# Kernel tuning notes

Measured on AMD Instinct MI355X. Metric: run time of the kernel, lower is better.

The kernel has to match this reference:

```python
import jax, jax.numpy as jnp
import numpy as np

D, T, HID, Q = 33, 49, 64, 64


def _lin(x, w, b):
    return x @ w.T + b


def setup_inputs() -> dict:
    key = jax.random.key(0)
    ks = jax.random.split(key, 40)

    def nrm(k, shape, scale=0.1):
        return jax.random.normal(k, shape, jnp.float32) * scale

    vals = nrm(ks[0], (D, T), 1.0)
    mask = (jax.random.uniform(ks[1], (D, T)) < 0.8).astype(jnp.float32)
    delta = jax.random.uniform(ks[2], (D, T)) * 2.0
    data = jnp.stack([vals, mask, delta])  # [3, 33, 49]

    return {
        "data": data,
        "h0": nrm(ks[3], (HID,), 1.0),
        "H0": nrm(ks[4], (D, HID), 1.0),
        "gh_w": nrm(ks[5], (HID, D)), "gh_b": nrm(ks[6], (HID,)),
        "gst_w": nrm(ks[7], (HID, D)), "gst_b": nrm(ks[8], (HID,)),
        "gru_wih": nrm(ks[9], (3 * HID, D)), "gru_whh": nrm(ks[10], (3 * HID, HID)),
        "gru_bih": nrm(ks[11], (3 * HID,)), "gru_bhh": nrm(ks[12], (3 * HID,)),
        "wu0_w": nrm(ks[13], (Q, HID)), "wu0_b": nrm(ks[14], (Q,)),
        "wu1_w": nrm(ks[15], (Q, 2 * HID)), "wu1_b": nrm(ks[16], (Q,)),
        "wu_w": nrm(ks[17], (Q, 3 * HID)), "wu_b": nrm(ks[18], (Q,)),
        "wh_w": nrm(ks[19], (D, HID + Q)), "wh_b": nrm(ks[20], (D,)),
        "xst_w": nrm(ks[21], (1, HID)), "xst_b": nrm(ks[22], (1,)),
        "wrg_w": nrm(ks[23], (D, HID)),
        "wrs": nrm(ks[24], (1, HID)),
        "tWz": nrm(ks[25], (D, HID, HID)), "tUzx": nrm(ks[26], (D, HID, 1)), "tUzh": nrm(ks[27], (D, HID, HID)),
        "tWr": nrm(ks[28], (D, HID, HID)), "tUrx": nrm(ks[29], (D, HID, 1)), "tUrh": nrm(ks[30], (D, HID, HID)),
        "tWh": nrm(ks[31], (D, HID, HID)), "tUhx": nrm(ks[32], (D, HID, 1)), "tUhh": nrm(ks[33], (D, HID, HID)),
        "tbz": nrm(ks[34], (HID, 1)), "tbr": nrm(ks[35], (HID, 1)), "tbh": nrm(ks[36], (HID, 1)),
    }


def reference(data, h0, H0, gh_w, gh_b, gst_w, gst_b, gru_wih, gru_whh,
              gru_bih, gru_bhh, wu0_w, wu0_b, wu1_w, wu1_b, wu_w, wu_b,
              wh_w, wh_b, xst_w, xst_b, wrg_w, wrs, tWz, tUzx, tUzh,
              tWr, tUrx, tUrh, tWh, tUhx, tUhh, tbz, tbr, tbh):
    X, M, Dt = data[0], data[1], data[2]  # each (33, 49)
    h = h0          # (HID,) -> becomes (1, HID) after first GRUCell step
    H = H0          # (D, HID)
    outs, Hs, xps = [], [], []
    for t in range(T):
        x, m, d = X[:, t], M[:, t], Dt[:, t]
        # GRU-D style decay gate: exp(-max(0, Linear(delta)))
        gamma_h = jnp.exp(-jax.nn.relu(_lin(d, gh_w, gh_b)))
        h = gamma_h * h
        x_st = _lin(H, xst_w, xst_b).reshape(-1)       # (D,)
        x_st_c = m * x + (1 - m) * x_st                # imputed input
        # torch nn.GRUCell
        xi = x_st_c.reshape(1, D)
        hi = h.reshape(1, HID)
        gi = _lin(xi, gru_wih, gru_bih)
        gh_ = _lin(hi, gru_whh, gru_bhh)
        i_r, i_z, i_n = jnp.split(gi, 3, axis=1)
        h_r, h_z, h_n = jnp.split(gh_, 3, axis=1)
        r = jax.nn.sigmoid(i_r + h_r)
        z = jax.nn.sigmoid(i_z + h_z)
        n = jnp.tanh(i_n + r * h_n)
        h = (1 - z) * n + z * hi                       # (1, HID)
        # original detaches the history used for u_t
        outs.append(jax.lax.stop_gradient(h))
        if t == 0:
            u_t = _lin(h0.reshape(1, -1), wu0_w, wu0_b)
        elif t == 1:
            hd = jnp.concatenate([h0.reshape(1, -1), outs[0]], 0).reshape(1, -1)
            u_t = _lin(hd, wu1_w, wu1_b)
        elif t == 2:
            hd = jnp.concatenate([h0.reshape(1, -1), outs[0], outs[1]], 0).reshape(1, -1)
            u_t = _lin(hd, wu_w, wu_b)
        else:
            hd = jnp.concatenate(outs[t - 3:t], 0).reshape(1, -1)
            u_t = _lin(hd, wu_w, wu_b)
        x_gt_hat = _lin(jnp.concatenate([h, u_t], axis=1), wh_w, wh_b)  # (1, D)
        gamma_st = jnp.exp(-jax.nn.relu(_lin(d, gst_w, gst_b)))
        H = gamma_st * H
        # tMGRU cell: per-variable (D=33) batched matmuls
        Hr = H[:, :, None]              # (D, HID, 1)
        xr = x_st_c[:, None, None]      # (D, 1, 1)
        hr = h.reshape(HID, 1)          # (HID, 1)
        z_t = jax.nn.sigmoid(tWz @ Hr + tUzx @ xr + tUzh @ hr + tbz)
        r_t = jax.nn.sigmoid(tWr @ Hr + tUrx @ xr + tUrh @ hr + tbr)
        Hh = jnp.tanh(r_t * (tWh @ Hr) + tUhx @ xr + tUhh @ hr + tbh)
        H = (z_t * Hr + (1 - z_t) * Hh).reshape(D, HID)
        Hs.append(H)
        a = h @ wrg_w.T                 # (1, D)
        b = wrs @ H.T                   # (1, D)
        alpha1 = jax.nn.softmax(a / (a + b), axis=-1)
        alpha2 = jax.nn.softmax(b / (a + b), axis=-1)
        xps.append(alpha1 * x_gt_hat + alpha2 * x_st)  # (1, D)
    H_s = jnp.stack(Hs)                         # (T, D, HID)
    x_pred = jnp.concatenate(xps, axis=0).T     # (D, T)
    return H_s, x_pred
```

## Files before the change

### kernel.cpp

```cpp
#include <hip/hip_runtime.h>
#include <math.h>

#define DD 33
#define TT 49
#define HH 64
#define NB 33
#define NT 256

#define O_WIHT  0
#define O_WHHT  6336
#define O_GH    18624
#define O_GS    21760
#define O_WT0   24896
#define O_WT1   27008
#define O_WTG   31232
#define O_CU    37568
#define O_XC    37700
#define O_R     39317
#define O_FLAGS 42560
#define PREP_N  37700

#define SC_AGENT __HIP_MEMORY_SCOPE_AGENT

__device__ __forceinline__ float sigm(float x) { return 1.f / (1.f + expf(-x)); }

__device__ __forceinline__ float rsum64(float v) {
#pragma unroll
  for (int o = 32; o > 0; o >>= 1) v += __shfl_xor(v, o, 64);
  return v;
}
__device__ __forceinline__ float rmax64(float v) {
#pragma unroll
  for (int o = 32; o > 0; o >>= 1) v = fmaxf(v, __shfl_xor(v, o, 64));
  return v;
}

extern "C" __global__ void gmgru_prep(
    const float* __restrict__ data, const float* __restrict__ gh_w,
    const float* __restrict__ gh_b, const float* __restrict__ gst_w,
    const float* __restrict__ gst_b, const float* __restrict__ wih,
    const float* __restrict__ whh, const float* __restrict__ wu0,
    const float* __restrict__ wu0b, const float* __restrict__ wu1,
    const float* __restrict__ wu1b, const float* __restrict__ wu,
    const float* __restrict__ wub, const float* __restrict__ wh_w,
    float* __restrict__ ws) {
  int idx = blockIdx.x * blockDim.x + threadIdx.x;
  if (idx < 6336) {
    int k = idx / 192, j = idx % 192;
    ws[O_WIHT + idx] = wih[j * DD + k];
  } else if (idx < 18624) {
    int r = idx - 6336, k = r / 192, j = r % 192;
    ws[O_WHHT + r] = whh[j * HH + k];
  } else if (idx < 21760) {
    int r = idx - 18624, t = r / 64, i = r % 64;
    float s = gh_b[i];
    for (int d2 = 0; d2 < DD; ++d2)
      s += data[2 * DD * TT + d2 * TT + t] * gh_w[i * DD + d2];
    ws[O_GH + r] = expf(-fmaxf(s, 0.f));
  } else if (idx < 24896) {
    int r = idx - 21760, t = r / 64, i = r % 64;
    float s = gst_b[i];
    for (int d2 = 0; d2 < DD; ++d2)
      s += data[2 * DD * TT + d2 * TT + t] * gst_w[i * DD + d2];
    ws[O_GS + r] = expf(-fmaxf(s, 0.f));
  } else if (idx < 27008) {
    int r = idx - 24896, dd = r / 64, k = r % 64;
    float s = 0.f;
    for (int q = 0; q < 64; ++q) s += wu0[q * 64 + k] * wh_w[dd * 128 + 64 + q];
    ws[O_WT0 + r] = s;
  } else if (idx < 31232) {
    int r = idx - 27008, dd = r / 128, k = r % 128;
    float s = 0.f;
    for (int q = 0; q < 64; ++q) s += wu1[q * 128 + k] * wh_w[dd * 128 + 64 + q];
    ws[O_WT1 + r] = s;
  } else if (idx < 37568) {
    int r = idx - 31232, dd = r / 192, k = r % 192;
    float s = 0.f;
    for (int q = 0; q < 64; ++q) s += wu[q * 192 + k] * wh_w[dd * 128 + 64 + q];
    ws[O_WTG + r] = s;
  } else if (idx < PREP_N) {
    int r = idx - 37568, dd = r / 4, v = r % 4;
    float s = 0.f;
    if (v < 3) {
      const float* bp = (v == 0) ? wu0b : (v == 1) ? wu1b : wub;
      for (int q = 0; q < 64; ++q) s += bp[q] * wh_w[dd * 128 + 64 + q];
    }
    ws[O_CU + r] = s;
  }
}

extern "C" __global__ void __launch_bounds__(NT)
gmgru_main(const float* __restrict__ data, const float* __restrict__ h0,
           const float* __restrict__ H0, const float* __restrict__ bih,
           const float* __restrict__ bhh, const float* __restrict__ wh_w,
           const float* __restrict__ wh_b, const float* __restrict__ xst_w,
           const float* __restrict__ xst_b, const float* __restrict__ wrg_w,
           const float* __restrict__ wrs, const float* __restrict__ tWz,
           const float* __restrict__ tUzx, const float* __restrict__ tUzh,
           const float* __restrict__ tWr, const float* __restrict__ tUrx,
           const float* __restrict__ tUrh, const float* __restrict__ tWh,
           const float* __restrict__ tUhx, const float* __restrict__ tUhh,
           const float* __restrict__ tbz, const float* __restrict__ tbr,
           const float* __restrict__ tbh, float* __restrict__ ws,
           unsigned* __restrict__ flags, float* __restrict__ out) {
  __shared__ __attribute__((aligned(16))) float ubuf[3][4096];
  __shared__ float whhT_l[12288];
  __shared__ float wihT_l[6336];
  __shared__ float partW[3][4][HH], partU[3][4][HH];
  __shared__ float ux[3][HH], tbl[3][HH];
  __shared__ float Hrow[HH], Hdec[HH], hpre[HH], hprev[HH], hnew_l[HH], h0s[HH];
  __shared__ float hist[4][HH];
  __shared__ float ghL[3 * HH];
  __shared__ float bihL[3 * HH], bhhL[3 * HH];
  __shared__ float whr0[HH], wtgL[192], wt0L[HH], wt1L[128];
  __shared__ float wrgr[HH], wrsr[HH], xstwL[HH];
  __shared__ float xrow[TT], mrow[TT];
  __shared__ float gpre[2][HH];
  __shared__ float scal2[2][2];

  const int tid = threadIdx.x;
  const int dd = blockIdx.x;
  const int wid = tid >> 6;
  const int lane = tid & 63;

  {
    const float* usrc[3] = {tUzh, tUrh, tUhh};
#pragma unroll 1
    for (int m = 0; m < 3; ++m) {
      const float* s = usrc[m] + dd * 4096;
#pragma unroll
      for (int c = 0; c < 4; ++c) {
        int f = tid * 16 + c * 4;
        float4 v = *reinterpret_cast<const float4*>(s + f);
        int i = f >> 6, k = f & 63;
        *reinterpret_cast<float4*>(&ubuf[m][(k >> 2) * 256 + i * 4]) = v;
      }
    }
  }
  for (int i = tid; i < 12288; i += NT) whhT_l[i] = ws[O_WHHT + i];
  for (int i = tid; i < 6336; i += NT) wihT_l[i] = ws[O_WIHT + i];
  if (tid < 192) {
    bihL[tid] = bih[tid];
    bhhL[tid] = bhh[tid];
    wtgL[tid] = ws[O_WTG + dd * 192 + tid];
  }
  if (tid < 128) wt1L[tid] = ws[O_WT1 + dd * 128 + tid];
  if (tid < HH) {
    ux[0][tid] = tUzx[dd * HH + tid];
    ux[1][tid] = tUrx[dd * HH + tid];
    ux[2][tid] = tUhx[dd * HH + tid];
    tbl[0][tid] = tbz[tid];
    tbl[1][tid] = tbr[tid];
    tbl[2][tid] = tbh[tid];
    Hrow[tid] = H0[dd * HH + tid];
    float h0v = h0[tid];
    h0s[tid] = h0v;
    hprev[tid] = h0v;
    whr0[tid] = wh_w[dd * 128 + tid];
    wt0L[tid] = ws[O_WT0 + dd * 64 + tid];
    wrgr[tid] = wrg_w[dd * HH + tid];
    wrsr[tid] = wrs[tid];
    xstwL[tid] = xst_w[tid];
    gpre[0][tid] = ws[O_GH + tid];
    gpre[1][tid] = ws[O_GS + tid];
  }
  if (tid < TT) {
    xrow[tid] = data[dd * TT + tid];
    mrow[tid] = data[DD * TT + dd * TT + tid];
  }
  const float whb_r = wh_b[dd];
  const float xstb_r = xst_b[0];
  const float cu0_r = ws[O_CU + dd * 4 + 0];
  const float cu1_r = ws[O_CU + dd * 4 + 1];
  const float cu2_r = ws[O_CU + dd * 4 + 2];
  __syncthreads();

  float xst_cur = 0.f;
  if (wid == 0) {
    float s = rsum64(Hrow[lane] * xstwL[lane]);
    if (lane == 0) {
      float xstv = s + xstb_r;
      xst_cur = xstv;
      float xcv = mrow[0] * xrow[0] + (1.f - mrow[0]) * xstv;
      __hip_atomic_store(&ws[O_XC + dd], xcv, __ATOMIC_RELAXED, SC_AGENT);
      asm volatile("s_waitcnt vmcnt(0)" ::: "memory");
      __hip_atomic_store(&flags[dd], 1u, __ATOMIC_RELAXED, SC_AGENT);
    }
  }

  for (int t = 0; t < TT; ++t) {
    __syncthreads();
    if (tid < HH) {
      hpre[tid] = gpre[0][tid] * hprev[tid];
      Hdec[tid] = gpre[1][tid] * Hrow[tid];
    }
    __syncthreads();

    {
      float Hv[16];
#pragma unroll
      for (int j = 0; j < 16; ++j) Hv[j] = Hdec[wid * 16 + j];
      float pw0 = 0.f, pw1 = 0.f, pw2 = 0.f;
      const int base = dd * 4096 + lane * 64 + wid * 16;
#pragma unroll
      for (int g = 0; g < 4; ++g) {
        float4 a = *reinterpret_cast<const float4*>(tWz + base + g * 4);
        float4 b = *reinterpret_cast<const float4*>(tWr + base + g * 4);
        float4 c = *reinterpret_cast<const float4*>(tWh + base + g * 4);
        const float h0v = Hv[g * 4 + 0], h1v = Hv[g * 4 + 1];
        const float h2v = Hv[g * 4 + 2], h3v = Hv[g * 4 + 3];
        pw0 += a.x * h0v + a.y * h1v + a.z * h2v + a.w * h3v;
        pw1 += b.x * h0v + b.y * h1v + b.z * h2v + b.w * h3v;
        pw2 += c.x * h0v + c.y * h1v + c.z * h2v + c.w * h3v;
      }
      partW[0][wid][lane] = pw0;
      partW[1][wid][lane] = pw1;
      partW[2][wid][lane] = pw2;
    }
    if (tid < 3 * HH) {
      float a0 = 0.f, a1 = 0.f, a2 = 0.f, a3 = 0.f;
#pragma unroll
      for (int k = 0; k < HH; k += 4) {
        a0 += whhT_l[(k + 0) * 192 + tid] * hpre[k + 0];
        a1 += whhT_l[(k + 1) * 192 + tid] * hpre[k + 1];
        a2 += whhT_l[(k + 2) * 192 + tid] * hpre[k + 2];
        a3 += whhT_l[(k + 3) * 192 + tid] * hpre[k + 3];
      }
      ghL[tid] = bhhL[tid] + ((a0 + a1) + (a2 + a3));
    }

    float hn = 0.f, xcv_reg = 0.f;
    if (wid == 0) {
      const unsigned tgt = (unsigned)(t + 1);
      while (true) {
        unsigned v = (lane < NB)
            ? __hip_atomic_load(&flags[lane], __ATOMIC_RELAXED, SC_AGENT)
            : 0xFFFFFFFFu;
        if (__all((int)(v >= tgt))) break;
        __builtin_amdgcn_s_sleep(1);
      }
      asm volatile("" ::: "memory");
      float xcv = 0.f;
      if (lane < DD)
        xcv = __hip_atomic_load(&ws[O_XC + t * DD + lane], __ATOMIC_RELAXED,
                                SC_AGENT);
      xcv_reg = xcv;
      float gr = bihL[lane], gz = bihL[64 + lane], gn = bihL[128 + lane];
      for (int k = 0; k < DD; ++k) {
        float xk = __shfl(xcv, k, 64);
        gr += wihT_l[k * 192 + lane] * xk;
        gz += wihT_l[k * 192 + 64 + lane] * xk;
        gn += wihT_l[k * 192 + 128 + lane] * xk;
      }
      float r = sigm(gr + ghL[lane]);
      float z = sigm(gz + ghL[64 + lane]);
      float n = tanhf(gn + r * ghL[128 + lane]);
      hn = (1.f - z) * n + z * hpre[lane];
      hnew_l[lane] = hn;
      hist[t & 3][lane] = hn;
      hprev[lane] = hn;
    }
    __syncthreads();

    {
      float hv[16];
#pragma unroll
      for (int j = 0; j < 16; ++j) hv[j] = hnew_l[wid * 16 + j];
      float pu0 = 0.f, pu1 = 0.f, pu2 = 0.f;
#pragma unroll
      for (int g = 0; g < 4; ++g) {
        const int kg = (wid * 4 + g) * 256 + lane * 4;
        float4 a = *reinterpret_cast<const float4*>(&ubuf[0][kg]);
        float4 b = *reinterpret_cast<const float4*>(&ubuf[1][kg]);
        float4 c = *reinterpret_cast<const float4*>(&ubuf[2][kg]);
        const float h0v = hv[g * 4 + 0], h1v = hv[g * 4 + 1];
        const float h2v = hv[g * 4 + 2], h3v = hv[g * 4 + 3];
        pu0 += a.x * h0v + a.y * h1v + a.z * h2v + a.w * h3v;
        pu1 += b.x * h0v + b.y * h1v + b.z * h2v + b.w * h3v;
        pu2 += c.x * h0v + c.y * h1v + c.z * h2v + c.w * h3v;
      }
      partU[0][wid][lane] = pu0;
      partU[1][wid][lane] = pu1;
      partU[2][wid][lane] = pu2;
    }
    __syncthreads();

    if (wid == 0) {
      float sz = partW[0][0][lane] + partW[0][1][lane] + partW[0][2][lane] +
                 partW[0][3][lane] + partU[0][0][lane] + partU[0][1][lane] +
                 partU[0][2][lane] + partU[0][3][lane];
      float sr = partW[1][0][lane] + partW[1][1][lane] + partW[1][2][lane] +
                 partW[1][3][lane] + partU[1][0][lane] + partU[1][1][lane] +
                 partU[1][2][lane] + partU[1][3][lane];
      float swh = partW[2][0][lane] + partW[2][1][lane] + partW[2][2][lane] +
                  partW[2][3][lane];
      float suh = partU[2][0][lane] + partU[2][1][lane] + partU[2][2][lane] +
                  partU[2][3][lane];
      float xc = __shfl(xcv_reg, dd, 64);
      float z = sigm(sz + ux[0][lane] * xc + tbl[0][lane]);
      float r = sigm(sr + ux[1][lane] * xc + tbl[1][lane]);
      float hh = tanhf(r * swh + ux[2][lane] * xc + suh + tbl[2][lane]);
      float Hn = z * Hdec[lane] + (1.f - z) * hh;
      Hrow[lane] = Hn;
      out[t * DD * HH + dd * HH + lane] = Hn;
      float xg = whr0[lane] * hn;
      if (t == 0) {
        xg += wt0L[lane] * h0s[lane];
      } else if (t == 1) {
        xg += wt1L[lane] * h0s[lane] + wt1L[64 + lane] * hist[0][lane];
      } else if (t == 2) {
        xg += wtgL[lane] * h0s[lane] + wtgL[64 + lane] * hist[0][lane] +
              wtgL[128 + lane] * hist[1][lane];
      } else {
        const int s0 = (t - 3) & 3, s1 = (t - 2) & 3, s2 = (t - 1) & 3;
        xg += wtgL[lane] * hist[s0][lane] + wtgL[64 + lane] * hist[s1][lane] +
              wtgL[128 + lane] * hist[s2][lane];
      }
      float xgt = rsum64(xg);
      float av = rsum64(wrgr[lane] * hn);
      float bv = rsum64(wrsr[lane] * Hn);
      float xsn = rsum64(xstwL[lane] * Hn);
      if (lane == 0) {
        float cu = (t == 0) ? cu0_r : (t == 1) ? cu1_r : cu2_r;
        scal2[t & 1][0] = xgt + whb_r + cu;
        scal2[t & 1][1] = xst_cur;
        float s = av + bv;
        __hip_atomic_store(&ws[O_R + t * 66 + dd], av / s, __ATOMIC_RELAXED,
                           SC_AGENT);
        __hip_atomic_store(&ws[O_R + t * 66 + 33 + dd], bv / s,
                           __ATOMIC_RELAXED, SC_AGENT);
        if (t < TT - 1) {
          float xstv = xsn + xstb_r;
          float xcn = mrow[t + 1] * xrow[t + 1] + (1.f - mrow[t + 1]) * xstv;
          __hip_atomic_store(&ws[O_XC + (t + 1) * DD + dd], xcn,
                             __ATOMIC_RELAXED, SC_AGENT);
          xst_cur = xstv;
        }
        asm volatile("s_waitcnt vmcnt(0)" ::: "memory");
        __hip_atomic_store(&flags[dd], (unsigned)(t + 2), __ATOMIC_RELAXED,
                           SC_AGENT);
      }
    } else if (wid == 1) {
      if (t > 0) {
        float r1v = -INFINITY, r2v = -INFINITY;
        if (lane < DD) {
          r1v = __hip_atomic_load(&ws[O_R + (t - 1) * 66 + lane],
                                  __ATOMIC_RELAXED, SC_AGENT);
          r2v = __hip_atomic_load(&ws[O_R + (t - 1) * 66 + 33 + lane],
                                  __ATOMIC_RELAXED, SC_AGENT);
        }
        float m1 = rmax64(r1v), m2 = rmax64(r2v);
        float e1 = (lane < DD) ? expf(r1v - m1) : 0.f;
        float e2 = (lane < DD) ? expf(r2v - m2) : 0.f;
        float s1 = rsum64(e1), s2 = rsum64(e2);
        float r1o = __shfl(r1v, dd, 64);
        float r2o = __shfl(r2v, dd, 64);
        if (lane == 0) {
          float a1 = expf(r1o - m1) / s1;
          float a2 = expf(r2o - m2) / s2;
          out[TT * DD * HH + dd * TT + (t - 1)] =
              a1 * scal2[(t - 1) & 1][0] + a2 * scal2[(t - 1) & 1][1];
        }
      }
    } else if (wid == 2) {
      if (t + 1 < TT) {
        gpre[0][lane] = ws[O_GH + (t + 1) * HH + lane];
        gpre[1][lane] = ws[O_GS + (t + 1) * HH + lane];
      }
    }
  }

  if (wid == 0) {
    const unsigned tgt = (unsigned)(TT + 1);
    while (true) {
      unsigned v = (lane < NB)
          ? __hip_atomic_load(&flags[lane], __ATOMIC_RELAXED, SC_AGENT)
          : 0xFFFFFFFFu;
      if (__all((int)(v >= tgt))) break;
      __builtin_amdgcn_s_sleep(1);
    }
    asm volatile("" ::: "memory");
  }
  __syncthreads();
  if (wid == 1) {
    float r1v = -INFINITY, r2v = -INFINITY;
    if (lane < DD) {
      r1v = __hip_atomic_load(&ws[O_R + (TT - 1) * 66 + lane], __ATOMIC_RELAXED,
                              SC_AGENT);
      r2v = __hip_atomic_load(&ws[O_R + (TT - 1) * 66 + 33 + lane],
                              __ATOMIC_RELAXED, SC_AGENT);
    }
    float m1 = rmax64(r1v), m2 = rmax64(r2v);
    float e1 = (lane < DD) ? expf(r1v - m1) : 0.f;
    float e2 = (lane < DD) ? expf(r2v - m2) : 0.f;
    float s1 = rsum64(e1), s2 = rsum64(e2);
    float r1o = __shfl(r1v, dd, 64);
    float r2o = __shfl(r2v, dd, 64);
    if (lane == 0) {
      float a1 = expf(r1o - m1) / s1;
      float a2 = expf(r2o - m2) / s2;
      out[TT * DD * HH + dd * TT + (TT - 1)] =
          a1 * scal2[(TT - 1) & 1][0] + a2 * scal2[(TT - 1) & 1][1];
    }
  }
}

extern "C" void kernel_launch(void* const* d_in, const int* in_sizes, int n_in,
                              void* d_out, int out_size, void* d_ws,
                              size_t ws_size, hipStream_t stream) {
  (void)in_sizes; (void)n_in; (void)out_size; (void)ws_size;
  const float* data   = (const float*)d_in[0];
  const float* h0     = (const float*)d_in[1];
  const float* H0     = (const float*)d_in[2];
  const float* gh_w   = (const float*)d_in[3];
  const float* gh_b   = (const float*)d_in[4];
  const float* gst_w  = (const float*)d_in[5];
  const float* gst_b  = (const float*)d_in[6];
  const float* wih    = (const float*)d_in[7];
  const float* whh    = (const float*)d_in[8];
  const float* bih    = (const float*)d_in[9];
  const float* bhh    = (const float*)d_in[10];
  const float* wu0w   = (const float*)d_in[11];
  const float* wu0b   = (const float*)d_in[12];
  const float* wu1w   = (const float*)d_in[13];
  const float* wu1b   = (const float*)d_in[14];
  const float* wuw    = (const float*)d_in[15];
  const float* wub    = (const float*)d_in[16];
  const float* wh_w   = (const float*)d_in[17];
  const float* wh_b   = (const float*)d_in[18];
  const float* xst_w  = (const float*)d_in[19];
  const float* xst_b  = (const float*)d_in[20];
  const float* wrg_w  = (const float*)d_in[21];
  const float* wrs    = (const float*)d_in[22];
  const float* tWz    = (const float*)d_in[23];
  const float* tUzx   = (const float*)d_in[24];
  const float* tUzh   = (const float*)d_in[25];
  const float* tWr    = (const float*)d_in[26];
  const float* tUrx   = (const float*)d_in[27];
  const float* tUrh   = (const float*)d_in[28];
  const float* tWh    = (const float*)d_in[29];
  const float* tUhx   = (const float*)d_in[30];
  const float* tUhh   = (const float*)d_in[31];
  const float* tbz    = (const float*)d_in[32];
  const float* tbr    = (const float*)d_in[33];
  const float* tbh    = (const float*)d_in[34];

  float* ws = (float*)d_ws;
  unsigned* flags = (unsigned*)(ws + O_FLAGS);

  hipMemsetAsync(flags, 0, 64 * sizeof(unsigned), stream);
  gmgru_prep<<<(PREP_N + 255) / 256, 256, 0, stream>>>(
      data, gh_w, gh_b, gst_w, gst_b, wih, whh, wu0w, wu0b, wu1w, wu1b, wuw,
      wub, wh_w, ws);
  gmgru_main<<<NB, NT, 0, stream>>>(
      data, h0, H0, bih, bhh, wh_w, wh_b, xst_w, xst_b, wrg_w, wrs, tWz, tUzx,
      tUzh, tWr, tUrx, tUrh, tWh, tUhx, tUhh, tbz, tbr, tbh, ws, flags,
      (float*)d_out);
}
```

Before: 220.5 us.

## Pack value and tag into 64-bit flags and keep per-step state in registers

Replaces the separate flag array plus value store with one 64-bit word per step per block that carries both the tag and the value. A single relaxed atomic load now both synchronises and delivers the data, so the separate fence and flag store disappear. The GRU cell is computed redundantly by every wave, with state held in registers and shuffles instead of shared memory, which cuts a __syncthreads per step. The softmax output is delayed by one extra step so its wait on remote data overlaps other work. It also preloads all gamma values into LDS, reads W_hh from global memory instead of LDS, and switches to fast exp/tanh, trading some accuracy and more global traffic for lower latency on the critical path.

```diff
diff --git a/kernel.cpp b/kernel.cpp
--- a/kernel.cpp
+++ b/kernel.cpp
@@ -15,14 +15,20 @@
 #define O_WT1   27008
 #define O_WTG   31232
 #define O_CU    37568
-#define O_XC    37700
-#define O_R     39317
-#define O_FLAGS 42560
+#define O_R     37700
+#define O_PF    40936
 #define PREP_N  37700
 
 #define SC_AGENT __HIP_MEMORY_SCOPE_AGENT
 
-__device__ __forceinline__ float sigm(float x) { return 1.f / (1.f + expf(-x)); }
+__device__ __forceinline__ float sigm(float x) {
+  return 1.f / (1.f + __expf(-x));
+}
+__device__ __forceinline__ float ftanh(float x) {
+  x = fminf(fmaxf(x, -15.f), 15.f);
+  float e = __expf(2.f * x);
+  return (e - 1.f) / (e + 1.f);
+}
 
 __device__ __forceinline__ float rsum64(float v) {
 #pragma unroll
@@ -89,7 +95,7 @@
   }
 }
 
-extern "C" __global__ void __launch_bounds__(NT)
+extern "C" __global__ void __launch_bounds__(NT, 1)
 gmgru_main(const float* __restrict__ data, const float* __restrict__ h0,
            const float* __restrict__ H0, const float* __restrict__ bih,
            const float* __restrict__ bhh, const float* __restrict__ wh_w,
@@ -102,21 +108,14 @@
            const float* __restrict__ tUhx, const float* __restrict__ tUhh,
            const float* __restrict__ tbz, const float* __restrict__ tbr,
            const float* __restrict__ tbh, float* __restrict__ ws,
-           unsigned* __restrict__ flags, float* __restrict__ out) {
+           unsigned long long* __restrict__ pf, float* __restrict__ out) {
   __shared__ __attribute__((aligned(16))) float ubuf[3][4096];
-  __shared__ float whhT_l[12288];
   __shared__ float wihT_l[6336];
-  __shared__ float partW[3][4][HH], partU[3][4][HH];
-  __shared__ float ux[3][HH], tbl[3][HH];
-  __shared__ float Hrow[HH], Hdec[HH], hpre[HH], hprev[HH], hnew_l[HH], h0s[HH];
-  __shared__ float hist[4][HH];
-  __shared__ float ghL[3 * HH];
-  __shared__ float bihL[3 * HH], bhhL[3 * HH];
-  __shared__ float whr0[HH], wtgL[192], wt0L[HH], wt1L[128];
-  __shared__ float wrgr[HH], wrsr[HH], xstwL[HH];
+  __shared__ float gamH[TT * HH], gamS[TT * HH];
+  __shared__ float part[2][6][4][HH];
+  __shared__ float hpreL[HH];
+  __shared__ float ghLDS[3 * HH];
   __shared__ float xrow[TT], mrow[TT];
-  __shared__ float gpre[2][HH];
-  __shared__ float scal2[2][2];
 
   const int tid = threadIdx.x;
   const int dd = blockIdx.x;
@@ -137,270 +136,273 @@
       }
     }
   }
-  for (int i = tid; i < 12288; i += NT) whhT_l[i] = ws[O_WHHT + i];
   for (int i = tid; i < 6336; i += NT) wihT_l[i] = ws[O_WIHT + i];
-  if (tid < 192) {
-    bihL[tid] = bih[tid];
-    bhhL[tid] = bhh[tid];
-    wtgL[tid] = ws[O_WTG + dd * 192 + tid];
-  }
-  if (tid < 128) wt1L[tid] = ws[O_WT1 + dd * 128 + tid];
-  if (tid < HH) {
-    ux[0][tid] = tUzx[dd * HH + tid];
-    ux[1][tid] = tUrx[dd * HH + tid];
-    ux[2][tid] = tUhx[dd * HH + tid];
-    tbl[0][tid] = tbz[tid];
-    tbl[1][tid] = tbr[tid];
-    tbl[2][tid] = tbh[tid];
-    Hrow[tid] = H0[dd * HH + tid];
-    float h0v = h0[tid];
-    h0s[tid] = h0v;
-    hprev[tid] = h0v;
-    whr0[tid] = wh_w[dd * 128 + tid];
-    wt0L[tid] = ws[O_WT0 + dd * 64 + tid];
-    wrgr[tid] = wrg_w[dd * HH + tid];
-    wrsr[tid] = wrs[tid];
-    xstwL[tid] = xst_w[tid];
-    gpre[0][tid] = ws[O_GH + tid];
-    gpre[1][tid] = ws[O_GS + tid];
+  for (int i = tid; i < TT * HH; i += NT) {
+    gamH[i] = ws[O_GH + i];
+    gamS[i] = ws[O_GS + i];
   }
   if (tid < TT) {
     xrow[tid] = data[dd * TT + tid];
     mrow[tid] = data[DD * TT + dd * TT + tid];
   }
-  const float whb_r = wh_b[dd];
-  const float xstb_r = xst_b[0];
+  const float bih_r = bih[lane];
+  const float bih_z = bih[64 + lane];
+  const float bih_n = bih[128 + lane];
+  const float bhh_r = (tid < 192) ? bhh[tid] : 0.f;
+  const float ux0 = tUzx[dd * HH + lane];
+  const float ux1 = tUrx[dd * HH + lane];
+  const float ux2 = tUhx[dd * HH + lane];
+  const float tb0 = tbz[lane];
+  const float tb1 = tbr[lane];
+  const float tb2 = tbh[lane];
+  const float xstw_r = xst_w[lane];
+  const float wrg_r = wrg_w[dd * HH + lane];
+  const float wrs_r = wrs[lane];
+  const float whr0_r = wh_w[dd * 128 + lane];
+  const float wtg0_r = ws[O_WTG + dd * 192 + lane];
+  const float wtg1_r = ws[O_WTG + dd * 192 + 64 + lane];
+  const float wtg2_r = ws[O_WTG + dd * 192 + 128 + lane];
+  const float wt0_r = ws[O_WT0 + dd * 64 + lane];
+  const float wt1a_r = ws[O_WT1 + dd * 128 + lane];
+  const float wt1b_r = ws[O_WT1 + dd * 128 + 64 + lane];
   const float cu0_r = ws[O_CU + dd * 4 + 0];
   const float cu1_r = ws[O_CU + dd * 4 + 1];
   const float cu2_r = ws[O_CU + dd * 4 + 2];
+  const float whb_r = wh_b[dd];
+  const float xstb_r = xst_b[0];
+  const float h0s_r = h0[lane];
+  float hprev = h0s_r;
+  float Hrow = H0[dd * HH + lane];
   __syncthreads();
 
-  float xst_cur = 0.f;
-  if (wid == 0) {
-    float s = rsum64(Hrow[lane] * xstwL[lane]);
-    if (lane == 0) {
-      float xstv = s + xstb_r;
-      xst_cur = xstv;
-      float xcv = mrow[0] * xrow[0] + (1.f - mrow[0]) * xstv;
-      __hip_atomic_store(&ws[O_XC + dd], xcv, __ATOMIC_RELAXED, SC_AGENT);
-      asm volatile("s_waitcnt vmcnt(0)" ::: "memory");
-      __hip_atomic_store(&flags[dd], 1u, __ATOMIC_RELAXED, SC_AGENT);
-    }
-  }
+  float xst_cur = rsum64(Hrow * xstw_r) + xstb_r;
+  if (wid == 0 && lane == 0) {
+    float xc0 = mrow[0] * xrow[0] + (1.f - mrow[0]) * xst_cur;
+    unsigned long long pk0 =
+        (1ULL << 32) | (unsigned long long)__float_as_uint(xc0);
+    __hip_atomic_store(&pf[dd], pk0, __ATOMIC_RELAXED, SC_AGENT);
+  }
+  float xg_m1 = 0.f, xg_m2 = 0.f, xs_m1 = 0.f, xs_m2 = 0.f;
+  float h1 = 0.f, h2 = 0.f, h3 = 0.f;
 
   for (int t = 0; t < TT; ++t) {
+    const int b = t & 1;
+    float hpre_r = gamH[t * HH + lane] * hprev;
+    float Hdec_r = gamS[t * HH + lane] * Hrow;
+    if (wid == 0) hpreL[lane] = hpre_r;
     __syncthreads();
-    if (tid < HH) {
-      hpre[tid] = gpre[0][tid] * hprev[tid];
-      Hdec[tid] = gpre[1][tid] * Hrow[tid];
-    }
-    __syncthreads();
-
+    if (tid < 3 * HH) {
+      float a0 = 0.f, a1 = 0.f, a2 = 0.f, a3 = 0.f;
+#pragma unroll
+      for (int k = 0; k < HH; k += 4) {
+        a0 += ws[O_WHHT + (k + 0) * 192 + tid] * hpreL[k + 0];
+        a1 += ws[O_WHHT + (k + 1) * 192 + tid] * hpreL[k + 1];
+        a2 += ws[O_WHHT + (k + 2) * 192 + tid] * hpreL[k + 2];
+        a3 += ws[O_WHHT + (k + 3) * 192 + tid] * hpreL[k + 3];
+      }
+      ghLDS[tid] = bhh_r + ((a0 + a1) + (a2 + a3));
+    }
     {
-      float Hv[16];
-#pragma unroll
-      for (int j = 0; j < 16; ++j) Hv[j] = Hdec[wid * 16 + j];
       float pw0 = 0.f, pw1 = 0.f, pw2 = 0.f;
       const int base = dd * 4096 + lane * 64 + wid * 16;
 #pragma unroll
       for (int g = 0; g < 4; ++g) {
         float4 a = *reinterpret_cast<const float4*>(tWz + base + g * 4);
-        float4 b = *reinterpret_cast<const float4*>(tWr + base + g * 4);
+        float4 bb = *reinterpret_cast<const float4*>(tWr + base + g * 4);
         float4 c = *reinterpret_cast<const float4*>(tWh + base + g * 4);
-        const float h0v = Hv[g * 4 + 0], h1v = Hv[g * 4 + 1];
-        const float h2v = Hv[g * 4 + 2], h3v = Hv[g * 4 + 3];
-        pw0 += a.x * h0v + a.y * h1v + a.z * h2v + a.w * h3v;
-        pw1 += b.x * h0v + b.y * h1v + b.z * h2v + b.w * h3v;
-        pw2 += c.x * h0v + c.y * h1v + c.z * h2v + c.w * h3v;
-      }
-      partW[0][wid][lane] = pw0;
-      partW[1][wid][lane] = pw1;
-      partW[2][wid][lane] = pw2;
-    }
-    if (tid < 3 * HH) {
-      float a0 = 0.f, a1 = 0.f, a2 = 0.f, a3 = 0.f;
-#pragma unroll
-      for (int k = 0; k < HH; k += 4) {
-        a0 += whhT_l[(k + 0) * 192 + tid] * hpre[k + 0];
-        a1 += whhT_l[(k + 1) * 192 + tid] * hpre[k + 1];
-        a2 += whhT_l[(k + 2) * 192 + tid] * hpre[k + 2];
-        a3 += whhT_l[(k + 3) * 192 + tid] * hpre[k + 3];
-      }
-      ghL[tid] = bhhL[tid] + ((a0 + a1) + (a2 + a3));
-    }
-
-    float hn = 0.f, xcv_reg = 0.f;
-    if (wid == 0) {
-      const unsigned tgt = (unsigned)(t + 1);
-      while (true) {
-        unsigned v = (lane < NB)
-            ? __hip_atomic_load(&flags[lane], __ATOMIC_RELAXED, SC_AGENT)
-            : 0xFFFFFFFFu;
-        if (__all((int)(v >= tgt))) break;
+        float v0 = __shfl(Hdec_r, wid * 16 + g * 4 + 0, 64);
+        float v1 = __shfl(Hdec_r, wid * 16 + g * 4 + 1, 64);
+        float v2 = __shfl(Hdec_r, wid * 16 + g * 4 + 2, 64);
+        float v3 = __shfl(Hdec_r, wid * 16 + g * 4 + 3, 64);
+        pw0 += a.x * v0 + a.y * v1 + a.z * v2 + a.w * v3;
+        pw1 += bb.x * v0 + bb.y * v1 + bb.z * v2 + bb.w * v3;
+        pw2 += c.x * v0 + c.y * v1 + c.z * v2 + c.w * v3;
+      }
+      part[b][0][wid][lane] = pw0;
+      part[b][1][wid][lane] = pw1;
+      part[b][2][wid][lane] = pw2;
+    }
+    __syncthreads();
+
+    const unsigned tagv = (unsigned)(t + 1);
+    float xcv;
+    {
+      unsigned long long pk;
+      for (;;) {
+        pk = (lane < NB)
+                 ? __hip_atomic_load(&pf[(size_t)t * NB + lane],
+                                     __ATOMIC_RELAXED, SC_AGENT)
+                 : (((unsigned long long)tagv) << 32);
+        if (__all((int)((unsigned)(pk >> 32) == tagv))) break;
         __builtin_amdgcn_s_sleep(1);
       }
+      xcv = __uint_as_float((unsigned)(pk & 0xFFFFFFFFull));
       asm volatile("" ::: "memory");
-      float xcv = 0.f;
-      if (lane < DD)
-        xcv = __hip_atomic_load(&ws[O_XC + t * DD + lane], __ATOMIC_RELAXED,
-                                SC_AGENT);
-      xcv_reg = xcv;
-      float gr = bihL[lane], gz = bihL[64 + lane], gn = bihL[128 + lane];
-      for (int k = 0; k < DD; ++k) {
-        float xk = __shfl(xcv, k, 64);
-        gr += wihT_l[k * 192 + lane] * xk;
-        gz += wihT_l[k * 192 + 64 + lane] * xk;
-        gn += wihT_l[k * 192 + 128 + lane] * xk;
-      }
-      float r = sigm(gr + ghL[lane]);
-      float z = sigm(gz + ghL[64 + lane]);
-      float n = tanhf(gn + r * ghL[128 + lane]);
-      hn = (1.f - z) * n + z * hpre[lane];
-      hnew_l[lane] = hn;
-      hist[t & 3][lane] = hn;
-      hprev[lane] = hn;
-    }
-    __syncthreads();
+    }
+
+    float gr = bih_r, gz = bih_z, gn = bih_n;
+#pragma unroll
+    for (int k = 0; k < DD; ++k) {
+      float xk = __shfl(xcv, k, 64);
+      gr += wihT_l[k * 192 + lane] * xk;
+      gz += wihT_l[k * 192 + 64 + lane] * xk;
+      gn += wihT_l[k * 192 + 128 + lane] * xk;
+    }
+    float rg = sigm(gr + ghLDS[lane]);
+    float zg = sigm(gz + ghLDS[64 + lane]);
+    float ng = ftanh(gn + rg * ghLDS[128 + lane]);
+    float hn = (1.f - zg) * ng + zg * hpre_r;
 
     {
-      float hv[16];
-#pragma unroll
-      for (int j = 0; j < 16; ++j) hv[j] = hnew_l[wid * 16 + j];
       float pu0 = 0.f, pu1 = 0.f, pu2 = 0.f;
 #pragma unroll
       for (int g = 0; g < 4; ++g) {
         const int kg = (wid * 4 + g) * 256 + lane * 4;
         float4 a = *reinterpret_cast<const float4*>(&ubuf[0][kg]);
-        float4 b = *reinterpret_cast<const float4*>(&ubuf[1][kg]);
+        float4 bb = *reinterpret_cast<const float4*>(&ubuf[1][kg]);
         float4 c = *reinterpret_cast<const float4*>(&ubuf[2][kg]);
-        const float h0v = hv[g * 4 + 0], h1v = hv[g * 4 + 1];
-        const float h2v = hv[g * 4 + 2], h3v = hv[g * 4 + 3];
-        pu0 += a.x * h0v + a.y * h1v + a.z * h2v + a.w * h3v;
-        pu1 += b.x * h0v + b.y * h1v + b.z * h2v + b.w * h3v;
-        pu2 += c.x * h0v + c.y * h1v + c.z * h2v + c.w * h3v;
-      }
-      partU[0][wid][lane] = pu0;
-      partU[1][wid][lane] = pu1;
-      partU[2][wid][lane] = pu2;
+        float v0 = __shfl(hn, wid * 16 + g * 4 + 0, 64);
+        float v1 = __shfl(hn, wid * 16 + g * 4 + 1, 64);
+        float v2 = __shfl(hn, wid * 16 + g * 4 + 2, 64);
+        float v3 = __shfl(hn, wid * 16 + g * 4 + 3, 64);
+        pu0 += a.x * v0 + a.y * v1 + a.z * v2 + a.w * v3;
+        pu1 += bb.x * v0 + bb.y * v1 + bb.z * v2 + bb.w * v3;
+        pu2 += c.x * v0 + c.y * v1 + c.z * v2 + c.w * v3;
+      }
+      part[b][3][wid][lane] = pu0;
+      part[b][4][wid][lane] = pu1;
+      part[b][5][wid][lane] = pu2;
     }
     __syncthreads();
 
+    float r1v = -INFINITY, r2v = -INFINITY;
+    if (wid == 1 && t >= 2 && lane < DD) {
+      r1v = __hip_atomic_load(&ws[O_R + (t - 2) * 66 + lane], __ATOMIC_RELAXED,
+                              SC_AGENT);
+      r2v = __hip_atomic_load(&ws[O_R + (t - 2) * 66 + 33 + lane],
+                              __ATOMIC_RELAXED, SC_AGENT);
+    }
+
+    float sz = part[b][0][0][lane] + part[b][0][1][lane] + part[b][0][2][lane] +
+               part[b][0][3][lane] + part[b][3][0][lane] + part[b][3][1][lane] +
+               part[b][3][2][lane] + part[b][3][3][lane];
+    float sr = part[b][1][0][lane] + part[b][1][1][lane] + part[b][1][2][lane] +
+               part[b][1][3][lane] + part[b][4][0][lane] + part[b][4][1][lane] +
+               part[b][4][2][lane] + part[b][4][3][lane];
+    float swh = part[b][2][0][lane] + part[b][2][1][lane] +
+                part[b][2][2][lane] + part[b][2][3][lane];
+    float suh = part[b][5][0][lane] + part[b][5][1][lane] +
+                part[b][5][2][lane] + part[b][5][3][lane];
+    float xc = __shfl(xcv, dd, 64);
+    float z2 = sigm(sz + ux0 * xc + tb0);
+    float r2g = sigm(sr + ux1 * xc + tb1);
+    float hh = ftanh(r2g * swh + ux2 * xc + suh + tb2);
+    float Hn = z2 * Hdec_r + (1.f - z2) * hh;
+
     if (wid == 0) {
-      float sz = partW[0][0][lane] + partW[0][1][lane] + partW[0][2][lane] +
-                 partW[0][3][lane] + partU[0][0][lane] + partU[0][1][lane] +
-                 partU[0][2][lane] + partU[0][3][lane];
-      float sr = partW[1][0][lane] + partW[1][1][lane] + partW[1][2][lane] +
-                 partW[1][3][lane] + partU[1][0][lane] + partU[1][1][lane] +
-                 partU[1][2][lane] + partU[1][3][lane];
-      float swh = partW[2][0][lane] + partW[2][1][lane] + partW[2][2][lane] +
-                  partW[2][3][lane];
-      float suh = partU[2][0][lane] + partU[2][1][lane] + partU[2][2][lane] +
-                  partU[2][3][lane];
-      float xc = __shfl(xcv_reg, dd, 64);
-      float z = sigm(sz + ux[0][lane] * xc + tbl[0][lane]);
-      float r = sigm(sr + ux[1][lane] * xc + tbl[1][lane]);
-      float hh = tanhf(r * swh + ux[2][lane] * xc + suh + tbl[2][lane]);
-      float Hn = z * Hdec[lane] + (1.f - z) * hh;
-      Hrow[lane] = Hn;
-      out[t * DD * HH + dd * HH + lane] = Hn;
-      float xg = whr0[lane] * hn;
-      if (t == 0) {
-        xg += wt0L[lane] * h0s[lane];
-      } else if (t == 1) {
-        xg += wt1L[lane] * h0s[lane] + wt1L[64 + lane] * hist[0][lane];
-      } else if (t == 2) {
-        xg += wtgL[lane] * h0s[lane] + wtgL[64 + lane] * hist[0][lane] +
-              wtgL[128 + lane] * hist[1][lane];
-      } else {
-        const int s0 = (t - 3) & 3, s1 = (t - 2) & 3, s2 = (t - 1) & 3;
-        xg += wtgL[lane] * hist[s0][lane] + wtgL[64 + lane] * hist[s1][lane] +
-              wtgL[128 + lane] * hist[s2][lane];
-      }
-      float xgt = rsum64(xg);
-      float av = rsum64(wrgr[lane] * hn);
-      float bv = rsum64(wrsr[lane] * Hn);
-      float xsn = rsum64(xstwL[lane] * Hn);
-      if (lane == 0) {
-        float cu = (t == 0) ? cu0_r : (t == 1) ? cu1_r : cu2_r;
-        scal2[t & 1][0] = xgt + whb_r + cu;
-        scal2[t & 1][1] = xst_cur;
-        float s = av + bv;
-        __hip_atomic_store(&ws[O_R + t * 66 + dd], av / s, __ATOMIC_RELAXED,
-                           SC_AGENT);
-        __hip_atomic_store(&ws[O_R + t * 66 + 33 + dd], bv / s,
+      float xsn = rsum64(xstw_r * Hn);
+      if (lane == 0 && t < TT - 1) {
+        float xstv = xsn + xstb_r;
+        float xcn = mrow[t + 1] * xrow[t + 1] + (1.f - mrow[t + 1]) * xstv;
+        unsigned long long pkn =
+            (((unsigned long long)(unsigned)(t + 2)) << 32) |
+            (unsigned long long)__float_as_uint(xcn);
+        __hip_atomic_store(&pf[(size_t)(t + 1) * NB + dd], pkn,
                            __ATOMIC_RELAXED, SC_AGENT);
-        if (t < TT - 1) {
-          float xstv = xsn + xstb_r;
-          float xcn = mrow[t + 1] * xrow[t + 1] + (1.f - mrow[t + 1]) * xstv;
-          __hip_atomic_store(&ws[O_XC + (t + 1) * DD + dd], xcn,
-                             __ATOMIC_RELAXED, SC_AGENT);
-          xst_cur = xstv;
-        }
-        asm volatile("s_waitcnt vmcnt(0)" ::: "memory");
-        __hip_atomic_store(&flags[dd], (unsigned)(t + 2), __ATOMIC_RELAXED,
-                           SC_AGENT);
       }
     } else if (wid == 1) {
-      if (t > 0) {
-        float r1v = -INFINITY, r2v = -INFINITY;
-        if (lane < DD) {
-          r1v = __hip_atomic_load(&ws[O_R + (t - 1) * 66 + lane],
-                                  __ATOMIC_RELAXED, SC_AGENT);
-          r2v = __hip_atomic_load(&ws[O_R + (t - 1) * 66 + 33 + lane],
-                                  __ATOMIC_RELAXED, SC_AGENT);
-        }
+      if (t >= 2) {
         float m1 = rmax64(r1v), m2 = rmax64(r2v);
-        float e1 = (lane < DD) ? expf(r1v - m1) : 0.f;
-        float e2 = (lane < DD) ? expf(r2v - m2) : 0.f;
+        float e1 = (lane < DD) ? __expf(r1v - m1) : 0.f;
+        float e2 = (lane < DD) ? __expf(r2v - m2) : 0.f;
         float s1 = rsum64(e1), s2 = rsum64(e2);
         float r1o = __shfl(r1v, dd, 64);
         float r2o = __shfl(r2v, dd, 64);
         if (lane == 0) {
-          float a1 = expf(r1o - m1) / s1;
-          float a2 = expf(r2o - m2) / s2;
-          out[TT * DD * HH + dd * TT + (t - 1)] =
-              a1 * scal2[(t - 1) & 1][0] + a2 * scal2[(t - 1) & 1][1];
+          float a1 = __expf(r1o - m1) / s1;
+          float a2 = __expf(r2o - m2) / s2;
+          out[TT * DD * HH + dd * TT + (t - 2)] = a1 * xg_m2 + a2 * xs_m2;
         }
       }
+      float xg = whr0_r * hn;
+      if (t == 0) {
+        xg += wt0_r * h0s_r;
+      } else if (t == 1) {
+        xg += wt1a_r * h0s_r + wt1b_r * h1;
+      } else if (t == 2) {
+        xg += wtg0_r * h0s_r + wtg1_r * h2 + wtg2_r * h1;
+      } else {
+        xg += wtg0_r * h3 + wtg1_r * h2 + wtg2_r * h1;
+      }
+      float xgt = rsum64(xg);
+      float cu = (t == 0) ? cu0_r : (t == 1) ? cu1_r : cu2_r;
+      float xsn1 = rsum64(xstw_r * Hn);
+      xg_m2 = xg_m1;
+      xs_m2 = xs_m1;
+      xg_m1 = xgt + whb_r + cu;
+      xs_m1 = xst_cur;
+      xst_cur = xsn1 + xstb_r;
+      h3 = h2;
+      h2 = h1;
+      h1 = hn;
     } else if (wid == 2) {
-      if (t + 1 < TT) {
-        gpre[0][lane] = ws[O_GH + (t + 1) * HH + lane];
-        gpre[1][lane] = ws[O_GS + (t + 1) * HH + lane];
-      }
-    }
-  }
-
-  if (wid == 0) {
-    const unsigned tgt = (unsigned)(TT + 1);
-    while (true) {
-      unsigned v = (lane < NB)
-          ? __hip_atomic_load(&flags[lane], __ATOMIC_RELAXED, SC_AGENT)
-          : 0xFFFFFFFFu;
-      if (__all((int)(v >= tgt))) break;
+      float av = rsum64(wrg_r * hn);
+      float bvv = rsum64(wrs_r * Hn);
+      if (lane == 0) {
+        float s = av + bvv;
+        __hip_atomic_store(&ws[O_R + t * 66 + dd], av / s, __ATOMIC_RELAXED,
+                           SC_AGENT);
+        __hip_atomic_store(&ws[O_R + t * 66 + 33 + dd], bvv / s,
+                           __ATOMIC_RELAXED, SC_AGENT);
+      }
+      asm volatile("s_waitcnt vmcnt(0)" ::: "memory");
+    } else {
+      out[t * DD * HH + dd * HH + lane] = Hn;
+    }
+    hprev = hn;
+    Hrow = Hn;
+  }
+
+  __syncthreads();
+  if (wid == 0 && lane == 0) {
+    __hip_atomic_store(&pf[(size_t)TT * NB + dd],
+                       (((unsigned long long)(unsigned)(TT + 1)) << 32),
+                       __ATOMIC_RELAXED, SC_AGENT);
+  }
+  if (wid == 1) {
+    const unsigned tagv = (unsigned)(TT + 1);
+    for (;;) {
+      unsigned long long pk =
+          (lane < NB) ? __hip_atomic_load(&pf[(size_t)TT * NB + lane],
+                                          __ATOMIC_RELAXED, SC_AGENT)
+                      : (((unsigned long long)tagv) << 32);
+      if (__all((int)((unsigned)(pk >> 32) == tagv))) break;
       __builtin_amdgcn_s_sleep(1);
     }
     asm volatile("" ::: "memory");
-  }
-  __syncthreads();
-  if (wid == 1) {
-    float r1v = -INFINITY, r2v = -INFINITY;
-    if (lane < DD) {
-      r1v = __hip_atomic_load(&ws[O_R + (TT - 1) * 66 + lane], __ATOMIC_RELAXED,
-                              SC_AGENT);
-      r2v = __hip_atomic_load(&ws[O_R + (TT - 1) * 66 + 33 + lane],
-                              __ATOMIC_RELAXED, SC_AGENT);
-    }
-    float m1 = rmax64(r1v), m2 = rmax64(r2v);
-    float e1 = (lane < DD) ? expf(r1v - m1) : 0.f;
-    float e2 = (lane < DD) ? expf(r2v - m2) : 0.f;
-    float s1 = rsum64(e1), s2 = rsum64(e2);
-    float r1o = __shfl(r1v, dd, 64);
-    float r2o = __shfl(r2v, dd, 64);
-    if (lane == 0) {
-      float a1 = expf(r1o - m1) / s1;
-      float a2 = expf(r2o - m2) / s2;
-      out[TT * DD * HH + dd * TT + (TT - 1)] =
-          a1 * scal2[(TT - 1) & 1][0] + a2 * scal2[(TT - 1) & 1][1];
+#pragma unroll 1
+    for (int e = 0; e < 2; ++e) {
+      const int step = TT - 2 + e;
+      float r1v = -INFINITY, r2v = -INFINITY;
+      if (lane < DD) {
+        r1v = __hip_atomic_load(&ws[O_R + step * 66 + lane], __ATOMIC_RELAXED,
+                                SC_AGENT);
+        r2v = __hip_atomic_load(&ws[O_R + step * 66 + 33 + lane],
+                                __ATOMIC_RELAXED, SC_AGENT);
+      }
+      float m1 = rmax64(r1v), m2 = rmax64(r2v);
+      float e1 = (lane < DD) ? __expf(r1v - m1) : 0.f;
+      float e2 = (lane < DD) ? __expf(r2v - m2) : 0.f;
+      float s1 = rsum64(e1), s2 = rsum64(e2);
+      float r1o = __shfl(r1v, dd, 64);
+      float r2o = __shfl(r2v, dd, 64);
+      if (lane == 0) {
+        float a1 = __expf(r1o - m1) / s1;
+        float a2 = __expf(r2o - m2) / s2;
+        float xgv = (e == 0) ? xg_m2 : xg_m1;
+        float xsv = (e == 0) ? xs_m2 : xs_m1;
+        out[TT * DD * HH + dd * TT + step] = a1 * xgv + a2 * xsv;
+      }
     }
   }
 }
@@ -446,14 +448,14 @@
   const float* tbh    = (const float*)d_in[34];
 
   float* ws = (float*)d_ws;
-  unsigned* flags = (unsigned*)(ws + O_FLAGS);
-
-  hipMemsetAsync(flags, 0, 64 * sizeof(unsigned), stream);
+  unsigned long long* pf = (unsigned long long*)(ws + O_PF);
+
+  hipMemsetAsync(pf, 0, (size_t)(TT + 1) * NB * 8, stream);
   gmgru_prep<<<(PREP_N + 255) / 256, 256, 0, stream>>>(
       data, gh_w, gh_b, gst_w, gst_b, wih, whh, wu0w, wu0b, wu1w, wu1b, wuw,
       wub, wh_w, ws);
   gmgru_main<<<NB, NT, 0, stream>>>(
       data, h0, H0, bih, bhh, wh_w, wh_b, xst_w, xst_b, wrg_w, wrs, tWz, tUzx,
-      tUzh, tWr, tUrx, tUrh, tWh, tUhx, tUhh, tbz, tbr, tbh, ws, flags,
+      tUzh, tWr, tUrx, tUrh, tWh, tUhx, tUhh, tbz, tbr, tbh, ws, pf,
       (float*)d_out);
 }
```

Measured after the change: 311.9 us. +41.5%, slower.
